# Optimization experiments

Hardware: AMD Instinct MI355X
Metric: run time of the kernel (lower is better)

Reference implementation:

```python
import jax, jax.numpy as jnp
import numpy as np

NUM_EXPERTS = 64
TOP_K = 8
LOAD_EMA_DECAY = 0.999
BIAS_TEMPERATURE = 1.0
NOISE_STD = 0.01


def setup_inputs() -> dict:
    key = jax.random.key(0)
    k1, k2, k3, k4 = jax.random.split(key, 4)
    hidden_states = jax.random.normal(k1, (4, 4096, 2048), dtype=jnp.float32)
    router_w = jax.random.normal(k2, (NUM_EXPERTS, 2048), dtype=jnp.float32) * 0.02
    expert_loads = jax.random.uniform(k3, (NUM_EXPERTS,), dtype=jnp.float32)
    bias_strength = jnp.ones((1,), dtype=jnp.float32)
    noise = jax.random.normal(k4, (4 * 4096, NUM_EXPERTS), dtype=jnp.float32)
    return {
        "hidden_states": hidden_states,
        "router_w": router_w,
        "expert_loads": expert_loads,
        "bias_strength": bias_strength,
        "noise": noise,
    }


def reference(hidden_states, router_w, expert_loads, bias_strength, noise):
    # Training-mode forward with total_routed > 0 (adaptive bias active),
    # balance_loss_weight = 0 (aux_loss is None in the original).
    E = NUM_EXPERTS
    x = hidden_states.reshape(-1, hidden_states.shape[-1])  # [N, d]
    n_tokens = x.shape[0]

    # Router linear (no bias) + training noise
    logits = jnp.einsum("nd,ed->ne", x, router_w) + noise * NOISE_STD  # [N, E]

    # Adaptive load-based bias (core of aux-loss-free routing)
    q = expert_loads / jnp.clip(expert_loads.sum(), 1e-8)  # normalized loads
    t = 1.0 / E  # expected uniform load
    # F.kl_div(log q, t, reduction='sum') = sum_e t*(log t - log q_e)
    kl = jnp.sum(t * (jnp.log(t) - jnp.log(jnp.clip(q, 1e-8))))
    adaptive_strength = jax.nn.sigmoid(kl * 10.0)
    new_bias_strength = 0.9 * bias_strength[0] + 0.1 * adaptive_strength
    bias = jnp.tanh((q - t) * E) * BIAS_TEMPERATURE * new_bias_strength  # [E]
    logits = logits - bias[None, :]

    # Top-k selection + softmax gating over selected logits
    expert_weights, expert_indices = jax.lax.top_k(logits, TOP_K)  # [N, K]
    expert_weights = jax.nn.softmax(expert_weights, axis=-1)

    # EMA load-statistics update (scatter-add of gate weights per expert)
    batch_loads = jax.ops.segment_sum(
        expert_weights.reshape(-1), expert_indices.reshape(-1), num_segments=E
    ) / n_tokens
    new_expert_loads = LOAD_EMA_DECAY * expert_loads + (1.0 - LOAD_EMA_DECAY) * batch_loads

    return expert_indices, expert_weights, new_expert_loads, new_bias_strength
```

## Files before the change

kernel.cpp:

```cpp
#include <hip/hip_runtime.h>
#include <math.h>

#define NT 16384
#define DIM 2048
#define NE 64
#define TK 8

typedef _Float16 f16_t;
typedef _Float16 half8 __attribute__((ext_vector_type(8)));
typedef float floatx16 __attribute__((ext_vector_type(16)));

__global__ __launch_bounds__(256) void prep_kernel(const float* __restrict__ w,
                                                   const float* __restrict__ expert_loads,
                                                   const float* __restrict__ bias_strength,
                                                   float* __restrict__ ws_bias,
                                                   float* __restrict__ ws_batch,
                                                   f16_t* __restrict__ whi,
                                                   f16_t* __restrict__ wlo,
                                                   float* __restrict__ out_bias_strength) {
    if (blockIdx.x == 64) {
        int e = threadIdx.x;
        if (e < 64) {
            float load = expert_loads[e];
            float s = load;
            #pragma unroll
            for (int off = 32; off >= 1; off >>= 1) s += __shfl_xor(s, off, 64);
            s = fmaxf(s, 1e-8f);
            float q = load / s;
            const float t = 1.0f / 64.0f;
            float kl = t * (logf(t) - logf(fmaxf(q, 1e-8f)));
            #pragma unroll
            for (int off = 32; off >= 1; off >>= 1) kl += __shfl_xor(kl, off, 64);
            float as = 1.0f / (1.0f + expf(-10.0f * kl));
            float nbs = 0.9f * bias_strength[0] + 0.1f * as;
            ws_bias[e] = tanhf((q - t) * 64.0f) * nbs;
            ws_batch[e] = 0.0f;
            if (e == 0) out_bias_strength[0] = nbs;
        }
        return;
    }
    int idx = blockIdx.x * 256 + threadIdx.x;
    int lane = idx & 63;
    int tile = (idx >> 6) & 1;
    int c    = idx >> 7;
    int n = tile * 32 + (lane & 31);
    int k = c * 16 + (lane >> 5) * 8;
    const float* src = w + (size_t)n * DIM + k;
    float4 a = *(const float4*)src;
    float4 b = *(const float4*)(src + 4);
    float v[8] = {a.x, a.y, a.z, a.w, b.x, b.y, b.z, b.w};
    half8 h, l;
    #pragma unroll
    for (int j = 0; j < 8; ++j) {
        f16_t hh = (f16_t)v[j];
        h[j] = hh;
        l[j] = (f16_t)(v[j] - (float)hh);
    }
    *(half8*)(whi + (size_t)idx * 8) = h;
    *(half8*)(wlo + (size_t)idx * 8) = l;
}

__global__ __launch_bounds__(512, 4) void router_main(const float* __restrict__ x,
                                                      const f16_t* __restrict__ whi,
                                                      const f16_t* __restrict__ wlo,
                                                      const float* __restrict__ noise,
                                                      const float* __restrict__ ws_bias,
                                                      float* __restrict__ ws_batch,
                                                      float* __restrict__ out) {
    __shared__ float smem[17408];
    __shared__ float bias_sh[64];
    __shared__ float loads_sh[64];

    const int tid = threadIdx.x;
    const int wv  = tid >> 6;
    const int L   = tid & 63;
    const int r   = L & 31;
    const int kh  = L >> 5;
    const int token0 = blockIdx.x * 32;

    if (tid < 64) { bias_sh[tid] = ws_bias[tid]; loads_sh[tid] = 0.0f; }

    const half8* whi8 = (const half8*)whi;
    const half8* wlo8 = (const half8*)wlo;

    floatx16 acc0, acc1;
    #pragma unroll
    for (int i = 0; i < 16; ++i) { acc0[i] = 0.0f; acc1[i] = 0.0f; }

    auto STAGE = [&](int S) {
        const int b_ = S & 1;
        #pragma unroll
        for (int q = 0; q < 4; ++q) {
            const int row_ = wv + q * 8;
            const float* gsrc = x + (size_t)(token0 + row_) * DIM + S * 256 + L * 4;
            float* ldst = (float*)(smem + b_ * 8320 + row_ * 260);
            __builtin_amdgcn_global_load_lds(
                (const __attribute__((address_space(1))) unsigned int*)gsrc,
                (__attribute__((address_space(3))) unsigned int*)ldst,
                16, 0, 0);
        }
    };

    STAGE(0);

    #pragma unroll
    for (int s = 0; s < 8; ++s) {
        half8 bf[8];
        {
            const int c0 = s * 16 + wv * 2;
            const int i0 = (c0 * 2) * 64 + L;
            const int i1 = ((c0 + 1) * 2) * 64 + L;
            bf[0] = whi8[i0];      bf[1] = whi8[i0 + 64];
            bf[2] = wlo8[i0];      bf[3] = wlo8[i0 + 64];
            bf[4] = whi8[i1];      bf[5] = whi8[i1 + 64];
            bf[6] = wlo8[i1];      bf[7] = wlo8[i1 + 64];
        }
        if (s < 7) {
            STAGE(s + 1);
            asm volatile("s_waitcnt vmcnt(12)" ::: "memory");
        } else {
            asm volatile("s_waitcnt vmcnt(8)" ::: "memory");
        }
        __builtin_amdgcn_sched_barrier(0);
        __builtin_amdgcn_s_barrier();

        const float* xrow = smem + (s & 1) * 8320 + r * 260 + wv * 32 + kh * 8;
        #pragma unroll
        for (int cc = 0; cc < 2; ++cc) {
            float4 f0 = *(const float4*)(xrow + cc * 16);
            float4 f1 = *(const float4*)(xrow + cc * 16 + 4);
            float v[8] = {f0.x, f0.y, f0.z, f0.w, f1.x, f1.y, f1.z, f1.w};
            half8 ah, al;
            #pragma unroll
            for (int j = 0; j < 8; ++j) {
                f16_t hh = (f16_t)v[j];
                ah[j] = hh;
                al[j] = (f16_t)(v[j] - (float)hh);
            }
            acc0 = __builtin_amdgcn_mfma_f32_32x32x16_f16(ah, bf[cc * 4 + 0], acc0, 0, 0, 0);
            acc1 = __builtin_amdgcn_mfma_f32_32x32x16_f16(ah, bf[cc * 4 + 1], acc1, 0, 0, 0);
            acc0 = __builtin_amdgcn_mfma_f32_32x32x16_f16(al, bf[cc * 4 + 0], acc0, 0, 0, 0);
            acc1 = __builtin_amdgcn_mfma_f32_32x32x16_f16(al, bf[cc * 4 + 1], acc1, 0, 0, 0);
            acc0 = __builtin_amdgcn_mfma_f32_32x32x16_f16(ah, bf[cc * 4 + 2], acc0, 0, 0, 0);
            acc1 = __builtin_amdgcn_mfma_f32_32x32x16_f16(ah, bf[cc * 4 + 3], acc1, 0, 0, 0);
        }
        __builtin_amdgcn_s_barrier();
    }

    #pragma unroll
    for (int reg = 0; reg < 16; ++reg) {
        int row = (reg & 3) + 8 * (reg >> 2) + 4 * kh;
        smem[wv * 2176 + row * 68 + r]      = acc0[reg];
        smem[wv * 2176 + row * 68 + 32 + r] = acc1[reg];
    }
    __syncthreads();

    #pragma unroll
    for (int p = 0; p < 4; ++p) {
        int o = tid + p * 512;
        int t = o >> 6, e = o & 63;
        float sum = 0.0f;
        #pragma unroll
        for (int q = 0; q < 8; ++q) sum += smem[q * 2176 + t * 68 + e];
        sum += noise[(size_t)(token0 + t) * NE + e] * 0.01f - bias_sh[e];
        smem[t * 68 + e] = sum;
    }
    __syncthreads();

    if (tid < 32) {
        int t = tid;
        float tv[TK]; int ti_[TK];
        #pragma unroll
        for (int j = 0; j < TK; ++j) { tv[j] = -INFINITY; ti_[j] = 0; }
        for (int e = 0; e < NE; ++e) {
            float v = smem[t * 68 + e]; int id = e;
            #pragma unroll
            for (int j = 0; j < TK; ++j) {
                bool gt = v > tv[j];
                float nv = gt ? v : tv[j];
                int   ni = gt ? id : ti_[j];
                float ov = gt ? tv[j] : v;
                int   oi = gt ? ti_[j] : id;
                tv[j] = nv; ti_[j] = ni; v = ov; id = oi;
            }
        }
        float m = tv[0], ssum = 0.0f, wvv[TK];
        #pragma unroll
        for (int j = 0; j < TK; ++j) { wvv[j] = expf(tv[j] - m); ssum += wvv[j]; }
        float inv = 1.0f / ssum;
        size_t gt_ = (size_t)(token0 + t);
        #pragma unroll
        for (int j = 0; j < TK; ++j) {
            float wgt = wvv[j] * inv;
            out[gt_ * TK + j] = (float)ti_[j];
            out[(size_t)NT * TK + gt_ * TK + j] = wgt;
            atomicAdd(&loads_sh[ti_[j]], wgt);
        }
    }
    __syncthreads();
    if (tid < 64) atomicAdd(&ws_batch[tid], loads_sh[tid]);
}

__global__ __launch_bounds__(64) void finalize_kernel(const float* __restrict__ expert_loads,
                                                      const float* __restrict__ ws_batch,
                                                      float* __restrict__ out_loads) {
    int e = threadIdx.x;
    out_loads[e] = 0.999f * expert_loads[e] + 0.001f * (ws_batch[e] / (float)NT);
}

extern "C" void kernel_launch(void* const* d_in, const int* in_sizes, int n_in,
                              void* d_out, int out_size, void* d_ws, size_t ws_size,
                              hipStream_t stream) {
    const float* x     = (const float*)d_in[0];
    const float* rw    = (const float*)d_in[1];
    const float* loads = (const float*)d_in[2];
    const float* bs    = (const float*)d_in[3];
    const float* noise = (const float*)d_in[4];
    float* out = (float*)d_out;
    float* ws  = (float*)d_ws;
    float* ws_bias  = ws;
    float* ws_batch = ws + 64;
    f16_t* whi = (f16_t*)(ws + 128);
    f16_t* wlo = whi + (size_t)16384 * 8;

    prep_kernel<<<65, 256, 0, stream>>>(rw, loads, bs, ws_bias, ws_batch, whi, wlo,
                                        out + (size_t)NT * TK * 2 + NE);
    router_main<<<NT / 32, 512, 0, stream>>>(x, whi, wlo, noise, ws_bias, ws_batch, out);
    finalize_kernel<<<1, 64, 0, stream>>>(loads, ws_batch, out + (size_t)NT * TK * 2);
}
```

Before: 214.0 us.

## Load activations directly to registers and fold finalize into last block

The activation tile is now loaded straight from global memory into registers with one-step register prefetch, replacing the double-buffered global_load_lds staging and the per-stage barriers. The separate finalize kernel is removed: a global atomic counter lets the last finishing block compute the EMA load update. This is meant to cut barrier and LDS traffic in the main loop and one kernel launch. In exchange it loses LDS-based coalescing of the x rows, since each lane now reads 32-byte chunks at row stride, and it adds a threadfence plus a global atomic per block.

```diff
diff --git a/kernel.cpp b/kernel.cpp
--- a/kernel.cpp
+++ b/kernel.cpp
@@ -15,6 +15,7 @@
                                                    const float* __restrict__ bias_strength,
                                                    float* __restrict__ ws_bias,
                                                    float* __restrict__ ws_batch,
+                                                   unsigned int* __restrict__ ws_counter,
                                                    f16_t* __restrict__ whi,
                                                    f16_t* __restrict__ wlo,
                                                    float* __restrict__ out_bias_strength) {
@@ -35,7 +36,7 @@
             float nbs = 0.9f * bias_strength[0] + 0.1f * as;
             ws_bias[e] = tanhf((q - t) * 64.0f) * nbs;
             ws_batch[e] = 0.0f;
-            if (e == 0) out_bias_strength[0] = nbs;
+            if (e == 0) { out_bias_strength[0] = nbs; ws_counter[0] = 0u; }
         }
         return;
     }
@@ -66,10 +67,13 @@
                                                       const float* __restrict__ noise,
                                                       const float* __restrict__ ws_bias,
                                                       float* __restrict__ ws_batch,
+                                                      unsigned int* __restrict__ ws_counter,
+                                                      const float* __restrict__ expert_loads,
                                                       float* __restrict__ out) {
     __shared__ float smem[17408];
     __shared__ float bias_sh[64];
     __shared__ float loads_sh[64];
+    __shared__ int last_flag;
 
     const int tid = threadIdx.x;
     const int wv  = tid >> 6;
@@ -79,6 +83,7 @@
     const int token0 = blockIdx.x * 32;
 
     if (tid < 64) { bias_sh[tid] = ws_bias[tid]; loads_sh[tid] = 0.0f; }
+    if (tid == 0) last_flag = 0;
 
     const half8* whi8 = (const half8*)whi;
     const half8* wlo8 = (const half8*)wlo;
@@ -87,49 +92,33 @@
     #pragma unroll
     for (int i = 0; i < 16; ++i) { acc0[i] = 0.0f; acc1[i] = 0.0f; }
 
-    auto STAGE = [&](int S) {
-        const int b_ = S & 1;
-        #pragma unroll
-        for (int q = 0; q < 4; ++q) {
-            const int row_ = wv + q * 8;
-            const float* gsrc = x + (size_t)(token0 + row_) * DIM + S * 256 + L * 4;
-            float* ldst = (float*)(smem + b_ * 8320 + row_ * 260);
-            __builtin_amdgcn_global_load_lds(
-                (const __attribute__((address_space(1))) unsigned int*)gsrc,
-                (__attribute__((address_space(3))) unsigned int*)ldst,
-                16, 0, 0);
-        }
-    };
-
-    STAGE(0);
-
-    #pragma unroll
+    const float* abase = x + (size_t)(token0 + r) * DIM + wv * 32 + kh * 8;
+
+    float4 pa0 = *(const float4*)(abase);
+    float4 pa1 = *(const float4*)(abase + 4);
+    float4 pa2 = *(const float4*)(abase + 16);
+    float4 pa3 = *(const float4*)(abase + 20);
+
+    #pragma unroll 1
     for (int s = 0; s < 8; ++s) {
-        half8 bf[8];
+        float4 a0 = pa0, a1 = pa1, a2 = pa2, a3 = pa3;
+        if (s < 7) {
+            const float* nb = abase + (s + 1) * 256;
+            pa0 = *(const float4*)(nb);
+            pa1 = *(const float4*)(nb + 4);
+            pa2 = *(const float4*)(nb + 16);
+            pa3 = *(const float4*)(nb + 20);
+        }
+        const int c0 = s * 16 + wv * 2;
+        const int i0 = (c0 * 2) * 64 + L;
+        const int i1 = ((c0 + 1) * 2) * 64 + L;
+        half8 b0h = whi8[i0], b1h = whi8[i0 + 64];
+        half8 b0l = wlo8[i0], b1l = wlo8[i0 + 64];
+        half8 b2h = whi8[i1], b3h = whi8[i1 + 64];
+        half8 b2l = wlo8[i1], b3l = wlo8[i1 + 64];
+
         {
-            const int c0 = s * 16 + wv * 2;
-            const int i0 = (c0 * 2) * 64 + L;
-            const int i1 = ((c0 + 1) * 2) * 64 + L;
-            bf[0] = whi8[i0];      bf[1] = whi8[i0 + 64];
-            bf[2] = wlo8[i0];      bf[3] = wlo8[i0 + 64];
-            bf[4] = whi8[i1];      bf[5] = whi8[i1 + 64];
-            bf[6] = wlo8[i1];      bf[7] = wlo8[i1 + 64];
-        }
-        if (s < 7) {
-            STAGE(s + 1);
-            asm volatile("s_waitcnt vmcnt(12)" ::: "memory");
-        } else {
-            asm volatile("s_waitcnt vmcnt(8)" ::: "memory");
-        }
-        __builtin_amdgcn_sched_barrier(0);
-        __builtin_amdgcn_s_barrier();
-
-        const float* xrow = smem + (s & 1) * 8320 + r * 260 + wv * 32 + kh * 8;
-        #pragma unroll
-        for (int cc = 0; cc < 2; ++cc) {
-            float4 f0 = *(const float4*)(xrow + cc * 16);
-            float4 f1 = *(const float4*)(xrow + cc * 16 + 4);
-            float v[8] = {f0.x, f0.y, f0.z, f0.w, f1.x, f1.y, f1.z, f1.w};
+            float v[8] = {a0.x, a0.y, a0.z, a0.w, a1.x, a1.y, a1.z, a1.w};
             half8 ah, al;
             #pragma unroll
             for (int j = 0; j < 8; ++j) {
@@ -137,14 +126,29 @@
                 ah[j] = hh;
                 al[j] = (f16_t)(v[j] - (float)hh);
             }
-            acc0 = __builtin_amdgcn_mfma_f32_32x32x16_f16(ah, bf[cc * 4 + 0], acc0, 0, 0, 0);
-            acc1 = __builtin_amdgcn_mfma_f32_32x32x16_f16(ah, bf[cc * 4 + 1], acc1, 0, 0, 0);
-            acc0 = __builtin_amdgcn_mfma_f32_32x32x16_f16(al, bf[cc * 4 + 0], acc0, 0, 0, 0);
-            acc1 = __builtin_amdgcn_mfma_f32_32x32x16_f16(al, bf[cc * 4 + 1], acc1, 0, 0, 0);
-            acc0 = __builtin_amdgcn_mfma_f32_32x32x16_f16(ah, bf[cc * 4 + 2], acc0, 0, 0, 0);
-            acc1 = __builtin_amdgcn_mfma_f32_32x32x16_f16(ah, bf[cc * 4 + 3], acc1, 0, 0, 0);
-        }
-        __builtin_amdgcn_s_barrier();
+            acc0 = __builtin_amdgcn_mfma_f32_32x32x16_f16(ah, b0h, acc0, 0, 0, 0);
+            acc1 = __builtin_amdgcn_mfma_f32_32x32x16_f16(ah, b1h, acc1, 0, 0, 0);
+            acc0 = __builtin_amdgcn_mfma_f32_32x32x16_f16(al, b0h, acc0, 0, 0, 0);
+            acc1 = __builtin_amdgcn_mfma_f32_32x32x16_f16(al, b1h, acc1, 0, 0, 0);
+            acc0 = __builtin_amdgcn_mfma_f32_32x32x16_f16(ah, b0l, acc0, 0, 0, 0);
+            acc1 = __builtin_amdgcn_mfma_f32_32x32x16_f16(ah, b1l, acc1, 0, 0, 0);
+        }
+        {
+            float v[8] = {a2.x, a2.y, a2.z, a2.w, a3.x, a3.y, a3.z, a3.w};
+            half8 ah, al;
+            #pragma unroll
+            for (int j = 0; j < 8; ++j) {
+                f16_t hh = (f16_t)v[j];
+                ah[j] = hh;
+                al[j] = (f16_t)(v[j] - (float)hh);
+            }
+            acc0 = __builtin_amdgcn_mfma_f32_32x32x16_f16(ah, b2h, acc0, 0, 0, 0);
+            acc1 = __builtin_amdgcn_mfma_f32_32x32x16_f16(ah, b3h, acc1, 0, 0, 0);
+            acc0 = __builtin_amdgcn_mfma_f32_32x32x16_f16(al, b2h, acc0, 0, 0, 0);
+            acc1 = __builtin_amdgcn_mfma_f32_32x32x16_f16(al, b3h, acc1, 0, 0, 0);
+            acc0 = __builtin_amdgcn_mfma_f32_32x32x16_f16(ah, b2l, acc0, 0, 0, 0);
+            acc1 = __builtin_amdgcn_mfma_f32_32x32x16_f16(ah, b3l, acc1, 0, 0, 0);
+        }
     }
 
     #pragma unroll
@@ -199,13 +203,17 @@
     }
     __syncthreads();
     if (tid < 64) atomicAdd(&ws_batch[tid], loads_sh[tid]);
-}
-
-__global__ __launch_bounds__(64) void finalize_kernel(const float* __restrict__ expert_loads,
-                                                      const float* __restrict__ ws_batch,
-                                                      float* __restrict__ out_loads) {
-    int e = threadIdx.x;
-    out_loads[e] = 0.999f * expert_loads[e] + 0.001f * (ws_batch[e] / (float)NT);
+
+    __threadfence();
+    if (tid == 0) {
+        unsigned int prev = atomicAdd(ws_counter, 1u);
+        if (prev == (unsigned int)(NT / 32 - 1)) last_flag = 1;
+    }
+    __syncthreads();
+    if (last_flag && tid < 64) {
+        float bl = atomicAdd(&ws_batch[tid], 0.0f);
+        out[(size_t)NT * TK * 2 + tid] = 0.999f * expert_loads[tid] + 0.001f * (bl / (float)NT);
+    }
 }
 
 extern "C" void kernel_launch(void* const* d_in, const int* in_sizes, int n_in,
@@ -220,11 +228,12 @@
     float* ws  = (float*)d_ws;
     float* ws_bias  = ws;
     float* ws_batch = ws + 64;
-    f16_t* whi = (f16_t*)(ws + 128);
+    unsigned int* ws_counter = (unsigned int*)(ws + 128);
+    f16_t* whi = (f16_t*)(ws + 160);
     f16_t* wlo = whi + (size_t)16384 * 8;
 
-    prep_kernel<<<65, 256, 0, stream>>>(rw, loads, bs, ws_bias, ws_batch, whi, wlo,
+    prep_kernel<<<65, 256, 0, stream>>>(rw, loads, bs, ws_bias, ws_batch, ws_counter, whi, wlo,
                                         out + (size_t)NT * TK * 2 + NE);
-    router_main<<<NT / 32, 512, 0, stream>>>(x, whi, wlo, noise, ws_bias, ws_batch, out);
-    finalize_kernel<<<1, 64, 0, stream>>>(loads, ws_batch, out + (size_t)NT * TK * 2);
+    router_main<<<NT / 32, 512, 0, stream>>>(x, whi, wlo, noise, ws_bias, ws_batch, ws_counter,
+                                             loads, out);
 }
```

Measured after the change: 293.6 us. 37.2% more time.
